# Optimization experiments

Measured on AMD Instinct MI355X. Metric: run time of the kernel, lower is better.

## Reference

```python
import jax, jax.numpy as jnp
import numpy as np
from jax import lax

DIM = 1024
B, N = 4, 4096


def setup_inputs() -> dict:
    key = jax.random.key(0)
    k1, k2 = jax.random.split(key)
    x = jax.random.normal(k1, (B, N, DIM), dtype=jnp.float32)
    # Linear(dim, 3*dim, bias=False): weight stored as [3*dim, dim] (torch convention)
    w_qkva = jax.random.normal(k2, (3 * DIM, DIM), dtype=jnp.float32) * (DIM ** -0.5)
    gamma = jnp.ones((DIM,), dtype=jnp.float32)  # RMSNorm gain
    return {"x": x, "w_qkva": w_qkva, "gamma": gamma}


def _rmsnorm(x, gamma):
    # lucidrains RMSNorm: F.normalize(x, dim=-1) * sqrt(dim) * gamma
    scale = jnp.asarray(x.shape[-1], x.dtype) ** 0.5
    norm = jnp.sqrt(jnp.sum(x * x, axis=-1, keepdims=True))
    return x / jnp.maximum(norm, 1e-12) * scale * gamma


def reference(x, w_qkva, gamma):
    h = _rmsnorm(x, gamma)                                  # [b, n, d]
    qkva = jnp.einsum('bnd,ed->bne', h, w_qkva)             # [b, n, 3d]
    q, kv, a = jnp.split(qkva, 3, axis=-1)                  # each [b, n, d]
    a = jax.nn.sigmoid(a)

    def binary_operator(e_i, e_j):
        a_i, kv_i = e_i
        a_j, kv_j = e_j
        return (a_j * a_i, a_j * kv_i + kv_j)

    # gated linear recurrence over the sequence axis (elementwise per channel)
    _, y = lax.associative_scan(binary_operator, (a, kv), axis=1)
    return q * y                                            # [b, n, d]
```

## Files before the change

### kernel.cpp

```cpp
#include <hip/hip_runtime.h>
#include <hip/hip_bf16.h>

#define SEQ_N 4096
#define BATCH 4
#define DIM 1024
#define M_ROWS (BATCH * SEQ_N)
#define NCOLS (3 * DIM)
#define KDIM DIM
#define CHUNK_L 32
#define NCHUNK (SEQ_N / CHUNK_L)
#define NCHANNEL (BATCH * DIM)
#define GT 32

using short8 = __attribute__((ext_vector_type(8))) short;
using f32x4  = __attribute__((ext_vector_type(4))) float;

static __device__ __forceinline__ unsigned short f2bf(float f) {
    union { float f; unsigned u; } v; v.f = f;
    unsigned r = v.u + 0x7fffu + ((v.u >> 16) & 1u);
    return (unsigned short)(r >> 16);
}
static __device__ __forceinline__ float bf2f(unsigned short s) {
    union { unsigned u; float f; } v; v.u = ((unsigned)s) << 16;
    return v.f;
}
static __device__ __forceinline__ float sigm(float x) {
    return 1.f / (1.f + __expf(-x));
}

__global__ __launch_bounds__(256) void wconv_kernel(const float* __restrict__ in,
                                                    unsigned short* __restrict__ out,
                                                    int n4) {
    int i = blockIdx.x * 256 + threadIdx.x;
    if (i < n4) {
        float4 v = reinterpret_cast<const float4*>(in)[i];
        ushort4 o;
        o.x = f2bf(v.x); o.y = f2bf(v.y); o.z = f2bf(v.z); o.w = f2bf(v.w);
        reinterpret_cast<ushort4*>(out)[i] = o;
    }
}

__global__ __launch_bounds__(256) void rmsnorm_kernel(const float* __restrict__ x,
                                                      const float* __restrict__ gamma,
                                                      unsigned short* __restrict__ h) {
    const int row = blockIdx.x;
    const int tid = threadIdx.x;
    const float4 v = reinterpret_cast<const float4*>(x + (size_t)row * DIM)[tid];
    float ss = v.x * v.x + v.y * v.y + v.z * v.z + v.w * v.w;
#pragma unroll
    for (int off = 32; off >= 1; off >>= 1) ss += __shfl_xor(ss, off, 64);
    __shared__ float red[4];
    if ((tid & 63) == 0) red[tid >> 6] = ss;
    __syncthreads();
    const float tot = red[0] + red[1] + red[2] + red[3];
    const float scale = 32.0f / fmaxf(sqrtf(tot), 1e-12f);
    const float4 g = reinterpret_cast<const float4*>(gamma)[tid];
    ushort4 o;
    o.x = f2bf(v.x * scale * g.x);
    o.y = f2bf(v.y * scale * g.y);
    o.z = f2bf(v.z * scale * g.z);
    o.w = f2bf(v.w * scale * g.w);
    reinterpret_cast<ushort4*>(h + (size_t)row * DIM)[tid] = o;
}

__global__ __launch_bounds__(512, 2) void gemm256_kernel(const unsigned short* __restrict__ A,
                                                         const unsigned short* __restrict__ B,
                                                         unsigned short* __restrict__ C) {
    __shared__ __align__(16) unsigned short sA[4][256][32];
    __shared__ __align__(16) unsigned short sB[4][256][32];

    const int tid  = threadIdx.x;
    const int lane = tid & 63;
    const int wave = tid >> 6;

    const int orig = blockIdx.x;
    const int swz  = (orig & 7) * 96 + (orig >> 3);
    const int ntile = swz >> 6;
    const int mtile = swz & 63;
    const int row0 = mtile * 256;
    const int col0 = ntile * 256;

    const int wm = (wave >> 2) * 128;
    const int wn = (wave & 3) * 64;
    const int fr = lane & 15;
    const int kq = lane >> 4;

    const int srow = tid >> 2;
    const int scol = (tid & 3) * 8;
    const unsigned short* aSrc = A + (size_t)(row0 + srow) * KDIM + scol;
    const unsigned short* bSrc = B + (size_t)(col0 + srow) * KDIM + scol;
    unsigned short* sAf = &sA[0][0][0];
    unsigned short* sBf = &sB[0][0][0];
    const int sdst = tid * 8;

#define STAGE_A(bs, kt, u)                                                              \
    __builtin_amdgcn_global_load_lds(                                                   \
        (const __attribute__((address_space(1))) void*)(aSrc + (size_t)(u) * 128 * KDIM + (kt) * 32), \
        (__attribute__((address_space(3))) void*)(sAf + (bs) * 8192 + (u) * 4096 + sdst), 16, 0, 0);
#define STAGE_B(bs, kt, u)                                                              \
    __builtin_amdgcn_global_load_lds(                                                   \
        (const __attribute__((address_space(1))) void*)(bSrc + (size_t)(u) * 128 * KDIM + (kt) * 32), \
        (__attribute__((address_space(3))) void*)(sBf + (bs) * 8192 + (u) * 4096 + sdst), 16, 0, 0);

    f32x4 acc[8][4] = {};

    STAGE_A(0, 0, 0); STAGE_A(0, 0, 1); STAGE_B(0, 0, 0); STAGE_B(0, 0, 1);
    STAGE_A(1, 1, 0); STAGE_A(1, 1, 1); STAGE_B(1, 1, 0); STAGE_B(1, 1, 1);
    asm volatile("s_waitcnt vmcnt(4)" ::: "memory");
    __builtin_amdgcn_sched_barrier(0);
    __builtin_amdgcn_s_barrier();

    for (int t = 0; t < GT; ++t) {
        const int b  = t & 3;
        const int bs = (t + 2) & 3;
        const bool st = (t + 2 < GT);
        const unsigned short* sAb = sAf + b * 8192;
        const unsigned short* sBb = sBf + b * 8192;

        short8 bfr[4], afr[4];
#pragma unroll
        for (int j = 0; j < 4; ++j)
            bfr[j] = *reinterpret_cast<const short8*>(sBb + (wn + j * 16 + fr) * 32 + kq * 8);
#pragma unroll
        for (int i = 0; i < 4; ++i)
            afr[i] = *reinterpret_cast<const short8*>(sAb + (wm + i * 16 + fr) * 32 + kq * 8);
        if (st) { STAGE_A(bs, t + 2, 0); STAGE_A(bs, t + 2, 1); }
        __builtin_amdgcn_s_barrier();
        __builtin_amdgcn_s_setprio(1);
#pragma unroll
        for (int i = 0; i < 4; ++i)
#pragma unroll
            for (int j = 0; j < 4; ++j)
                acc[i][j] = __builtin_amdgcn_mfma_f32_16x16x32_bf16(afr[i], bfr[j], acc[i][j], 0, 0, 0);
        __builtin_amdgcn_s_setprio(0);
        __builtin_amdgcn_s_barrier();

        short8 afr2[4];
#pragma unroll
        for (int i = 0; i < 4; ++i)
            afr2[i] = *reinterpret_cast<const short8*>(sAb + (wm + 64 + i * 16 + fr) * 32 + kq * 8);
        if (st) { STAGE_B(bs, t + 2, 0); STAGE_B(bs, t + 2, 1); }
        __builtin_amdgcn_s_barrier();
        __builtin_amdgcn_s_setprio(1);
#pragma unroll
        for (int i = 0; i < 4; ++i)
#pragma unroll
            for (int j = 0; j < 4; ++j)
                acc[4 + i][j] = __builtin_amdgcn_mfma_f32_16x16x32_bf16(afr2[i], bfr[j], acc[4 + i][j], 0, 0, 0);
        __builtin_amdgcn_s_setprio(0);
        if (t < GT - 2) {
            asm volatile("s_waitcnt vmcnt(4)" ::: "memory");
        } else if (t == GT - 2) {
            asm volatile("s_waitcnt vmcnt(0)" ::: "memory");
        }
        __builtin_amdgcn_sched_barrier(0);
        __builtin_amdgcn_s_barrier();
    }
#undef STAGE_A
#undef STAGE_B

#pragma unroll
    for (int i = 0; i < 8; ++i) {
#pragma unroll
        for (int j = 0; j < 4; ++j) {
#pragma unroll
            for (int r = 0; r < 4; ++r) {
                int row = row0 + wm + i * 16 + kq * 4 + r;
                int col = col0 + wn + j * 16 + fr;
                C[(size_t)row * NCOLS + col] = f2bf(acc[i][j][r]);
            }
        }
    }
}

__global__ __launch_bounds__(256) void chunk_agg_kernel(const unsigned short* __restrict__ qkva,
                                                        float* __restrict__ Aagg,
                                                        float* __restrict__ Yagg) {
    const int c = blockIdx.x, b = blockIdx.y;
    const int d4 = threadIdx.x * 4;
    const unsigned short* base = qkva + ((size_t)b * SEQ_N + c * CHUNK_L) * NCOLS;
    float s[4] = {0.f, 0.f, 0.f, 0.f};
    float A[4] = {1.f, 1.f, 1.f, 1.f};
#pragma unroll 4
    for (int n = 0; n < CHUNK_L; ++n) {
        const ushort4 kvu = *reinterpret_cast<const ushort4*>(base + (size_t)n * NCOLS + DIM + d4);
        const ushort4 au  = *reinterpret_cast<const ushort4*>(base + (size_t)n * NCOLS + 2 * DIM + d4);
        const float kv[4] = {bf2f(kvu.x), bf2f(kvu.y), bf2f(kvu.z), bf2f(kvu.w)};
        const float av[4] = {bf2f(au.x),  bf2f(au.y),  bf2f(au.z),  bf2f(au.w)};
#pragma unroll
        for (int j = 0; j < 4; ++j) {
            const float a = sigm(av[j]);
            s[j] = fmaf(a, s[j], kv[j]);
            A[j] *= a;
        }
    }
    const int idx = c * NCHANNEL + b * DIM + d4;
    float4 Ao, Yo;
    Ao.x = A[0]; Ao.y = A[1]; Ao.z = A[2]; Ao.w = A[3];
    Yo.x = s[0]; Yo.y = s[1]; Yo.z = s[2]; Yo.w = s[3];
    *reinterpret_cast<float4*>(&Aagg[idx]) = Ao;
    *reinterpret_cast<float4*>(&Yagg[idx]) = Yo;
}

__global__ __launch_bounds__(256) void agg_scan_kernel(const float* __restrict__ Aagg,
                                                       const float* __restrict__ Yagg,
                                                       float* __restrict__ Sin) {
    const int ch = blockIdx.x * 256 + threadIdx.x;
    float s = 0.f;
#pragma unroll 8
    for (int c = 0; c < NCHUNK; ++c) {
        const float A = Aagg[c * NCHANNEL + ch];
        const float Y = Yagg[c * NCHANNEL + ch];
        Sin[c * NCHANNEL + ch] = s;
        s = fmaf(A, s, Y);
    }
}

__global__ __launch_bounds__(256) void apply_kernel(const unsigned short* __restrict__ qkva,
                                                    const float* __restrict__ Sin,
                                                    float* __restrict__ out) {
    const int c = blockIdx.x, b = blockIdx.y;
    const int d4 = threadIdx.x * 4;
    const unsigned short* base = qkva + ((size_t)b * SEQ_N + c * CHUNK_L) * NCOLS;
    float* obase = out + ((size_t)b * SEQ_N + c * CHUNK_L) * DIM;
    const float4 s0 = *reinterpret_cast<const float4*>(&Sin[c * NCHANNEL + b * DIM + d4]);
    float s[4] = {s0.x, s0.y, s0.z, s0.w};
#pragma unroll 2
    for (int n = 0; n < CHUNK_L; ++n) {
        const ushort4 qu  = *reinterpret_cast<const ushort4*>(base + (size_t)n * NCOLS + d4);
        const ushort4 kvu = *reinterpret_cast<const ushort4*>(base + (size_t)n * NCOLS + DIM + d4);
        const ushort4 au  = *reinterpret_cast<const ushort4*>(base + (size_t)n * NCOLS + 2 * DIM + d4);
        const float kv[4] = {bf2f(kvu.x), bf2f(kvu.y), bf2f(kvu.z), bf2f(kvu.w)};
        const float av[4] = {bf2f(au.x),  bf2f(au.y),  bf2f(au.z),  bf2f(au.w)};
        const float q[4]  = {bf2f(qu.x),  bf2f(qu.y),  bf2f(qu.z),  bf2f(qu.w)};
        float4 o;
#pragma unroll
        for (int j = 0; j < 4; ++j) {
            const float a = sigm(av[j]);
            s[j] = fmaf(a, s[j], kv[j]);
        }
        o.x = q[0] * s[0]; o.y = q[1] * s[1]; o.z = q[2] * s[2]; o.w = q[3] * s[3];
        *reinterpret_cast<float4*>(&obase[(size_t)n * DIM + d4]) = o;
    }
}

extern "C" void kernel_launch(void* const* d_in, const int* in_sizes, int n_in,
                              void* d_out, int out_size, void* d_ws, size_t ws_size,
                              hipStream_t stream) {
    const float* x     = (const float*)d_in[0];
    const float* w     = (const float*)d_in[1];
    const float* gamma = (const float*)d_in[2];
    float* out = (float*)d_out;

    char* ws = (char*)d_ws;
    unsigned short* wb   = (unsigned short*)(ws);
    unsigned short* h    = (unsigned short*)(ws + 6291456);
    unsigned short* qkva = (unsigned short*)(ws + 39845888);
    float* Aagg = (float*)(ws + 6291456);
    float* Yagg = (float*)(ws + 6291456 + 2097152);
    float* Sin  = (float*)(ws + 6291456 + 4194304);

    wconv_kernel<<<(NCOLS * KDIM / 4 + 255) / 256, 256, 0, stream>>>(w, wb, NCOLS * KDIM / 4);
    rmsnorm_kernel<<<M_ROWS, 256, 0, stream>>>(x, gamma, h);
    gemm256_kernel<<<(M_ROWS / 256) * (NCOLS / 256), 512, 0, stream>>>(h, wb, qkva);
    chunk_agg_kernel<<<dim3(NCHUNK, BATCH), 256, 0, stream>>>(qkva, Aagg, Yagg);
    agg_scan_kernel<<<NCHANNEL / 256, 256, 0, stream>>>(Aagg, Yagg, Sin);
    apply_kernel<<<dim3(NCHUNK, BATCH), 256, 0, stream>>>(qkva, Sin, out);
}
```

Baseline: 296.9 us.

## Swizzle GEMM LDS layout, fuse pre-kernels, halve scan chunk length

The weight bf16 conversion and the RMSNorm are merged into one launch, saving a kernel launch and letting the two overlap. The GEMM's LDS layout now XORs the k-quad index with row bits, which targets bank conflicts on the short8 fragment reads. The scan chunk length drops from 32 to 16, which doubles the number of blocks for the chunk-aggregate and apply kernels, and the workspace offsets grow to hold the larger aggregate arrays. The apply loop unroll also rises, at the cost of a longer sequential agg-scan over twice as many chunks.

```diff
diff --git a/kernel.cpp b/kernel.cpp
--- a/kernel.cpp
+++ b/kernel.cpp
@@ -7,7 +7,7 @@
 #define M_ROWS (BATCH * SEQ_N)
 #define NCOLS (3 * DIM)
 #define KDIM DIM
-#define CHUNK_L 32
+#define CHUNK_L 16
 #define NCHUNK (SEQ_N / CHUNK_L)
 #define NCHANNEL (BATCH * DIM)
 #define GT 32
@@ -28,23 +28,23 @@
     return 1.f / (1.f + __expf(-x));
 }
 
-__global__ __launch_bounds__(256) void wconv_kernel(const float* __restrict__ in,
-                                                    unsigned short* __restrict__ out,
-                                                    int n4) {
-    int i = blockIdx.x * 256 + threadIdx.x;
-    if (i < n4) {
-        float4 v = reinterpret_cast<const float4*>(in)[i];
+#define WCONV_BLOCKS 3072
+__global__ __launch_bounds__(256) void pre_kernel(const float* __restrict__ w,
+                                                  unsigned short* __restrict__ wb,
+                                                  const float* __restrict__ x,
+                                                  const float* __restrict__ gamma,
+                                                  unsigned short* __restrict__ h) {
+    const int bid = blockIdx.x;
+    const int tid = threadIdx.x;
+    if (bid < WCONV_BLOCKS) {
+        const int i = bid * 256 + tid;
+        float4 v = reinterpret_cast<const float4*>(w)[i];
         ushort4 o;
         o.x = f2bf(v.x); o.y = f2bf(v.y); o.z = f2bf(v.z); o.w = f2bf(v.w);
-        reinterpret_cast<ushort4*>(out)[i] = o;
-    }
-}
-
-__global__ __launch_bounds__(256) void rmsnorm_kernel(const float* __restrict__ x,
-                                                      const float* __restrict__ gamma,
-                                                      unsigned short* __restrict__ h) {
-    const int row = blockIdx.x;
-    const int tid = threadIdx.x;
+        reinterpret_cast<ushort4*>(wb)[i] = o;
+        return;
+    }
+    const int row = bid - WCONV_BLOCKS;
     const float4 v = reinterpret_cast<const float4*>(x + (size_t)row * DIM)[tid];
     float ss = v.x * v.x + v.y * v.y + v.z * v.z + v.w * v.w;
 #pragma unroll
@@ -84,9 +84,10 @@
     const int wn = (wave & 3) * 64;
     const int fr = lane & 15;
     const int kq = lane >> 4;
+    const int kqx = kq ^ ((fr >> 1) & 3);
 
     const int srow = tid >> 2;
-    const int scol = (tid & 3) * 8;
+    const int scol = ((tid & 3) ^ ((srow >> 1) & 3)) * 8;
     const unsigned short* aSrc = A + (size_t)(row0 + srow) * KDIM + scol;
     const unsigned short* bSrc = B + (size_t)(col0 + srow) * KDIM + scol;
     unsigned short* sAf = &sA[0][0][0];
@@ -120,10 +121,10 @@
         short8 bfr[4], afr[4];
 #pragma unroll
         for (int j = 0; j < 4; ++j)
-            bfr[j] = *reinterpret_cast<const short8*>(sBb + (wn + j * 16 + fr) * 32 + kq * 8);
-#pragma unroll
-        for (int i = 0; i < 4; ++i)
-            afr[i] = *reinterpret_cast<const short8*>(sAb + (wm + i * 16 + fr) * 32 + kq * 8);
+            bfr[j] = *reinterpret_cast<const short8*>(sBb + (wn + j * 16 + fr) * 32 + kqx * 8);
+#pragma unroll
+        for (int i = 0; i < 4; ++i)
+            afr[i] = *reinterpret_cast<const short8*>(sAb + (wm + i * 16 + fr) * 32 + kqx * 8);
         if (st) { STAGE_A(bs, t + 2, 0); STAGE_A(bs, t + 2, 1); }
         __builtin_amdgcn_s_barrier();
         __builtin_amdgcn_s_setprio(1);
@@ -138,7 +139,7 @@
         short8 afr2[4];
 #pragma unroll
         for (int i = 0; i < 4; ++i)
-            afr2[i] = *reinterpret_cast<const short8*>(sAb + (wm + 64 + i * 16 + fr) * 32 + kq * 8);
+            afr2[i] = *reinterpret_cast<const short8*>(sAb + (wm + 64 + i * 16 + fr) * 32 + kqx * 8);
         if (st) { STAGE_B(bs, t + 2, 0); STAGE_B(bs, t + 2, 1); }
         __builtin_amdgcn_s_barrier();
         __builtin_amdgcn_s_setprio(1);
@@ -225,7 +226,7 @@
     float* obase = out + ((size_t)b * SEQ_N + c * CHUNK_L) * DIM;
     const float4 s0 = *reinterpret_cast<const float4*>(&Sin[c * NCHANNEL + b * DIM + d4]);
     float s[4] = {s0.x, s0.y, s0.z, s0.w};
-#pragma unroll 2
+#pragma unroll 4
     for (int n = 0; n < CHUNK_L; ++n) {
         const ushort4 qu  = *reinterpret_cast<const ushort4*>(base + (size_t)n * NCOLS + d4);
         const ushort4 kvu = *reinterpret_cast<const ushort4*>(base + (size_t)n * NCOLS + DIM + d4);
@@ -257,11 +258,10 @@
     unsigned short* h    = (unsigned short*)(ws + 6291456);
     unsigned short* qkva = (unsigned short*)(ws + 39845888);
     float* Aagg = (float*)(ws + 6291456);
-    float* Yagg = (float*)(ws + 6291456 + 2097152);
-    float* Sin  = (float*)(ws + 6291456 + 4194304);
-
-    wconv_kernel<<<(NCOLS * KDIM / 4 + 255) / 256, 256, 0, stream>>>(w, wb, NCOLS * KDIM / 4);
-    rmsnorm_kernel<<<M_ROWS, 256, 0, stream>>>(x, gamma, h);
+    float* Yagg = (float*)(ws + 6291456 + 4194304);
+    float* Sin  = (float*)(ws + 6291456 + 8388608);
+
+    pre_kernel<<<WCONV_BLOCKS + M_ROWS, 256, 0, stream>>>(w, wb, x, gamma, h);
     gemm256_kernel<<<(M_ROWS / 256) * (NCOLS / 256), 512, 0, stream>>>(h, wb, qkva);
     chunk_agg_kernel<<<dim3(NCHUNK, BATCH), 256, 0, stream>>>(qkva, Aagg, Yagg);
     agg_scan_kernel<<<NCHANNEL / 256, 256, 0, stream>>>(Aagg, Yagg, Sin);
```

Result: no change. 294.3 us (-0.9%).
